# Optimization experiments

Measured on AMD Instinct MI355X. Metric: run time of the kernel, lower is better.

The kernel has to match this reference:

```python
import jax, jax.numpy as jnp
import numpy as np

B, S, D, H = 4, 2048, 1024, 16
HD = D // H  # head_dim = 64


def setup_inputs() -> dict:
    key = jax.random.key(0)
    ks = jax.random.split(key, 6)
    scale = 1.0 / np.sqrt(D)
    x = jax.random.normal(ks[0], (B, S, D), dtype=jnp.float32)
    mask = jax.random.bernoulli(ks[1], 0.9, (B, S, S))  # bool, True = keep
    wq = jax.random.normal(ks[2], (D, D), dtype=jnp.float32) * scale
    wk = jax.random.normal(ks[3], (D, D), dtype=jnp.float32) * scale
    wv = jax.random.normal(ks[4], (D, D), dtype=jnp.float32) * scale
    wo = jax.random.normal(ks[5], (D, D), dtype=jnp.float32) * scale
    return {"x": x, "mask": mask, "wq": wq, "wk": wk, "wv": wv, "wo": wo}


def reference(x, mask, wq, wk, wv, wo):
    bsz, seqlen, dim = x.shape
    # nn.Linear applies x @ W.T; weights here stored as [out, in]
    xq = (x @ wq.T).reshape(bsz, seqlen, H, HD)
    xk = (x @ wk.T).reshape(bsz, seqlen, H, HD)
    xv = (x @ wv.T).reshape(bsz, seqlen, H, HD)
    # scores: [B, H, S, S]
    scores = jnp.einsum("bqhd,bkhd->bhqk", xq, xk) / np.sqrt(HD).astype(np.float32)
    # additive mask: ~mask * -1e9, broadcast over heads
    neg = jnp.where(mask[:, None, :, :], 0.0, -1e9).astype(scores.dtype)
    scores = scores + neg
    scores = jax.nn.softmax(scores.astype(jnp.float32), axis=-1).astype(xq.dtype)
    # multiplicative re-mask after softmax (as in the original)
    scores = scores * mask[:, None, :, :].astype(scores.dtype)
    out = jnp.einsum("bhqk,bkhd->bqhd", scores, xv).reshape(bsz, seqlen, dim)
    return out @ wo.T
```

## Files before the change

### kernel.cpp

```cpp
#include <hip/hip_runtime.h>
#include <hip/hip_bf16.h>

#define S_LEN 2048
#define DIM   1024
#define NHEAD 16
#define HDIM  64
#define QSCALE 0.18033688f

typedef __attribute__((ext_vector_type(8))) short bfrag;
typedef __attribute__((ext_vector_type(4))) float f32x4;
typedef __attribute__((ext_vector_type(16))) float f32x16;
typedef __attribute__((ext_vector_type(4))) unsigned int u32x4;

#define MFMA(a,b,c)   __builtin_amdgcn_mfma_f32_16x16x32_bf16((a),(b),(c),0,0,0)
#define MFMA32(a,b,c) __builtin_amdgcn_mfma_f32_32x32x16_bf16((a),(b),(c),0,0,0)

__device__ __forceinline__ unsigned short f2bf(float x) {
  __hip_bfloat16 h = __float2bfloat16(x);
  return *reinterpret_cast<unsigned short*>(&h);
}

__device__ __forceinline__ unsigned int pk2bf(float a, float b) {
  float2 f2; f2.x = a; f2.y = b;
  __hip_bfloat162 b2 = __float22bfloat162_rn(f2);
  return *reinterpret_cast<unsigned int*>(&b2);
}

__device__ __forceinline__ void gll16(const unsigned short* g, unsigned short* l) {
  __builtin_amdgcn_global_load_lds(
      (const __attribute__((address_space(1))) unsigned int*)g,
      (__attribute__((address_space(3))) unsigned int*)l, 16, 0, 0);
}

__global__ void probe(const unsigned int* __restrict__ x,
                      const unsigned int* __restrict__ mask,
                      int* __restrict__ flags) {
  const int lane = threadIdx.x;
  int insane = 0;
  for (int i = lane; i < 512; i += 64) {
    unsigned int w = x[i];
    unsigned int e = (w >> 7) & 0xFFu;
    bool sane = (e >= 90u && e <= 160u) || ((w & 0x7FFFu) == 0u);
    insane += sane ? 0 : 1;
  }
  bool all01 = true, allu8 = true, allf32 = true, allbf = true;
  for (int i = lane; i < 1024; i += 64) {
    unsigned int w = mask[i];
    all01  &= (w <= 1u);
    allu8  &= ((w & 0xFEFEFEFEu) == 0u);
    allf32 &= (w == 0u || w == 0x3F800000u);
    unsigned int lo = w & 0xFFFFu, hi = w >> 16;
    allbf  &= (lo == 0u || lo == 0x3F80u) && (hi == 0u || hi == 0x3F80u);
  }
#pragma unroll
  for (int off = 1; off < 64; off <<= 1) insane += __shfl_xor(insane, off, 64);
  const unsigned long long full = ~0ull;
  const bool g01  = __ballot(all01)  == full;
  const bool gu8  = __ballot(allu8)  == full;
  const bool gf32 = __ballot(allf32) == full;
  const bool gbf  = __ballot(allbf)  == full;
  if (lane == 0) {
    flags[0] = (insane > 128) ? 1 : 0;
    flags[1] = g01 ? 1 : (gu8 ? 0 : (gf32 ? 2 : (gbf ? 3 : 0)));
  }
}

__device__ __forceinline__ bool mask_at(const void* mk, int mode, size_t idx) {
  switch (mode) {
    case 0:  return ((const unsigned char*)mk)[idx]  != 0;
    case 1:  return ((const int*)mk)[idx]            != 0;
    case 2:  return ((const unsigned int*)mk)[idx]   != 0u;
    default: return ((const unsigned short*)mk)[idx] != 0;
  }
}

__global__ __launch_bounds__(256) void cvt_all(
    const void* __restrict__ x,  const void* __restrict__ wq,
    const void* __restrict__ wk, const void* __restrict__ wv,
    const void* __restrict__ wo,
    unsigned short* __restrict__ xb,  unsigned short* __restrict__ wqb,
    unsigned short* __restrict__ wkb, unsigned short* __restrict__ wvb,
    unsigned short* __restrict__ wob, const int* __restrict__ flags) {
  const int bx = blockIdx.x;
  const void* src; unsigned short* dst; int i;
  if (bx < 4096) { src = x; dst = xb; i = bx * 256 + threadIdx.x; }
  else {
    const int r = (bx - 4096) >> 9, off = (bx - 4096) & 511;
    src = r == 0 ? wq : r == 1 ? wk : r == 2 ? wv : wo;
    dst = r == 0 ? wqb : r == 1 ? wkb : r == 2 ? wvb : wob;
    i = off * 256 + threadIdx.x;
  }
  if (flags[0]) {
    const float* p = (const float*)src + (size_t)i * 8;
    float4 a = *reinterpret_cast<const float4*>(p);
    float4 b = *reinterpret_cast<const float4*>(p + 4);
    unsigned int d0 = pk2bf(a.x, a.y), d1 = pk2bf(a.z, a.w);
    unsigned int d2 = pk2bf(b.x, b.y), d3 = pk2bf(b.z, b.w);
    uint4 o; o.x = d0; o.y = d1; o.z = d2; o.w = d3;
    *reinterpret_cast<uint4*>(dst + (size_t)i * 8) = o;
  } else {
    *reinterpret_cast<bfrag*>(dst + (size_t)i * 8) =
        reinterpret_cast<const bfrag*>(src)[i];
  }
}

__global__ __launch_bounds__(256) void bitmask(const void* __restrict__ mk,
                                               const int* __restrict__ flags,
                                               unsigned long long* __restrict__ mb) {
  size_t gid = (size_t)blockIdx.x * 256 + threadIdx.x;
  bool v = mask_at(mk, flags[1], gid);
  unsigned long long w = __ballot(v);
  if ((threadIdx.x & 63) == 0) {
    const size_t bb = gid >> 22;
    const size_t q  = (gid >> 11) & 2047;
    const size_t wd = (gid >> 6) & 31;
    mb[(bb * 32 + wd) * 2048 + q] = w;
  }
}

__global__ __launch_bounds__(256) void gemm128(const unsigned short* __restrict__ A,
                                               const unsigned short* __restrict__ Bt,
                                               void* __restrict__ C,
                                               const int* __restrict__ flags,
                                               int aHsplit, int cMode) {
  __shared__ unsigned short As[128 * 64];
  __shared__ unsigned short Bs[128 * 64];
  const int t = threadIdx.x, lane = t & 63, wave = t >> 6;
  const int r16 = lane & 15, quad = lane >> 4;

  const int nwgx = gridDim.x;
  const int nwg  = nwgx * gridDim.y;
  const int orig = blockIdx.y * nwgx + blockIdx.x;
  const int cpx  = nwg >> 3;
  const int swz  = (orig & 7) * cpx + (orig >> 3);
  const int n0 = (swz % nwgx) * 128, m0 = (swz / nwgx) * 128;

  const int wm = (wave >> 1) * 64, wn = (wave & 1) * 64;
  const int srow = t >> 3;
  const int sgr  = (t & 7) ^ (srow & 7);

  f32x4 acc[4][4];
#pragma unroll
  for (int i = 0; i < 4; ++i)
#pragma unroll
    for (int j = 0; j < 4; ++j) acc[i][j] = (f32x4){0.f, 0.f, 0.f, 0.f};

  for (int k0 = 0; k0 < 1024; k0 += 64) {
    __syncthreads();
#pragma unroll
    for (int rr = 0; rr < 4; ++rr) {
      const int row = rr * 32 + srow;
      const int m = m0 + row;
      const int k = k0 + sgr * 8;
      const unsigned short* ga;
      if (aHsplit) ga = A + ((size_t)(((m >> 11) << 4) + (k >> 6)) * 2048 + (m & 2047)) * 64 + (k & 63);
      else         ga = A + (size_t)m * 1024 + k;
      gll16(ga, As + rr * 2048 + wave * 512);
      const unsigned short* gb = Bt + (size_t)(n0 + row) * 1024 + k;
      gll16(gb, Bs + rr * 2048 + wave * 512);
    }
    __syncthreads();

#pragma unroll
    for (int kk = 0; kk < 2; ++kk) {
      bfrag af[4], bf[4];
#pragma unroll
      for (int i = 0; i < 4; ++i)
        af[i] = *reinterpret_cast<const bfrag*>(
            &As[(wm + i * 16 + r16) * 64 + (((kk * 4 + quad) ^ (r16 & 7)) * 8)]);
#pragma unroll
      for (int j = 0; j < 4; ++j)
        bf[j] = *reinterpret_cast<const bfrag*>(
            &Bs[(wn + j * 16 + r16) * 64 + (((kk * 4 + quad) ^ (r16 & 7)) * 8)]);
#pragma unroll
      for (int i = 0; i < 4; ++i)
#pragma unroll
        for (int j = 0; j < 4; ++j)
          acc[i][j] = MFMA(af[i], bf[j], acc[i][j]);
    }
  }

  const int oF = (cMode == 2) ? flags[0] : 0;
#pragma unroll
  for (int i = 0; i < 4; ++i)
#pragma unroll
    for (int j = 0; j < 4; ++j)
#pragma unroll
      for (int r = 0; r < 4; ++r) {
        const int m = m0 + wm + i * 16 + quad * 4 + r;
        const int n = n0 + wn + j * 16 + r16;
        const float v = acc[i][j][r];
        if (cMode == 3) {
          const int region = n >> 10, nn = n & 1023;
          const float vv = (region == 0) ? v * QSCALE : v;
          const size_t idx = (size_t)region * 8388608 +
              ((size_t)((m >> 11) * NHEAD + (nn >> 6)) * 2048 + (m & 2047)) * 64 + (nn & 63);
          ((unsigned short*)C)[idx] = f2bf(vv);
        } else if (cMode == 1) {
          const size_t idx = ((size_t)((m >> 11) * NHEAD + (n >> 6)) * 2048 + (m & 2047)) * 64 + (n & 63);
          ((unsigned short*)C)[idx] = f2bf(v);
        } else {
          const size_t idx = (size_t)m * 1024 + n;
          if (oF) ((float*)C)[idx] = v;
          else    ((unsigned short*)C)[idx] = f2bf(v);
        }
      }
}

__global__ __launch_bounds__(256) void transposeV(const unsigned short* __restrict__ xvH,
                                                  unsigned short* __restrict__ xvT) {
  __shared__ unsigned short Ts[64 * 80];
  const int t = threadIdx.x;
  const int s0 = blockIdx.x * 64, bh = blockIdx.y;
  const int sr = t >> 3, seg = (t & 7) * 8;
#pragma unroll
  for (int rr = 0; rr < 2; ++rr) {
    const int s = rr * 32 + sr;
    bfrag v = *reinterpret_cast<const bfrag*>(xvH + ((size_t)bh * 2048 + s0 + s) * 64 + seg);
#pragma unroll
    for (int j = 0; j < 8; ++j) Ts[(seg + j) * 80 + s] = (unsigned short)v[j];
  }
  __syncthreads();
#pragma unroll
  for (int rr = 0; rr < 2; ++rr) {
    const int d = rr * 32 + sr;
    bfrag o = *reinterpret_cast<const bfrag*>(&Ts[d * 80 + seg]);
    *reinterpret_cast<bfrag*>(xvT + ((size_t)bh * 64 + d) * 2048 + s0 + seg) = o;
  }
}

#if defined(__has_builtin)
#if __has_builtin(__builtin_amdgcn_permlane32_swap)
#define HAVE_PL32_SWAP 1
#endif
#endif
#ifndef HAVE_PL32_SWAP
#define HAVE_PL32_SWAP 0
#endif

__global__ __launch_bounds__(256, 3) void fattn(const unsigned short* __restrict__ qH,
                                                const unsigned short* __restrict__ kH,
                                                const unsigned short* __restrict__ vT,
                                                const unsigned long long* __restrict__ mbT,
                                                unsigned short* __restrict__ oH) {
  __shared__ unsigned short Ks[2][64 * 64];
  __shared__ unsigned short Vs[2][64 * 64];
  const int t = threadIdx.x, lane = t & 63, wave = t >> 6;
  const int l31 = lane & 31, hi = lane >> 5;
  const int bid = blockIdx.x;
  const int bh = bid & 63, qidx = bid >> 6;
  const int b = bh >> 4;
  const int qw = qidx * 128 + wave * 32;
  const size_t hbase = (size_t)bh * S_LEN;
  const int kgr = l31 & 7;

  bfrag qf[4];
#pragma unroll
  for (int s = 0; s < 4; ++s)
    qf[s] = *reinterpret_cast<const bfrag*>(
        qH + (hbase + qw + l31) * 64 + s * 16 + hi * 8);

  f32x16 o0, o1;
#pragma unroll
  for (int r = 0; r < 16; ++r) { o0[r] = 0.f; o1[r] = 0.f; }
  float ls[4] = {0.f, 0.f, 0.f, 0.f};

  const int srow = lane >> 3;
  const int sg   = (lane & 7) ^ srow;

  auto stage = [&](int buf, int kb) {
#pragma unroll
    for (int rr = 0; rr < 2; ++rr) {
      const int row = rr * 32 + wave * 8 + srow;
      gll16(kH + (hbase + kb + row) * 64 + sg * 8, &Ks[buf][rr * 2048 + wave * 512]);
      gll16(vT + ((size_t)bh * 64 + row) * 2048 + kb + sg * 8, &Vs[buf][rr * 2048 + wave * 512]);
    }
  };

  stage(0, 0);
  int cur = 0;
  const unsigned long long* mcol = mbT + (size_t)b * 32 * S_LEN + (qw + l31);
  unsigned long long wcur = mcol[0];

  for (int kb = 0; kb < S_LEN; kb += 64) {
    __syncthreads();
    const bool more = (kb + 64 < S_LEN);
    if (more) stage(cur ^ 1, kb + 64);
    const unsigned long long wnext =
        more ? mcol[(size_t)((kb >> 6) + 1) * S_LEN] : 0ull;

    const unsigned int wlo = (unsigned int)(wcur >> (4 * hi));
    const unsigned int whi = (unsigned int)(wcur >> (32 + 4 * hi));

#pragma unroll
    for (int c = 0; c < 2; ++c) {
      f32x16 z;
#pragma unroll
      for (int r = 0; r < 16; ++r) z[r] = 0.f;
      __builtin_amdgcn_s_setprio(1);
#pragma unroll
      for (int s = 0; s < 4; ++s) {
        const int gr = (2 * s + hi) ^ kgr;
        bfrag kf = *reinterpret_cast<const bfrag*>(
            &Ks[cur][(c * 32 + l31) * 64 + gr * 8]);
        z = MFMA32(kf, qf[s], z);
      }
      __builtin_amdgcn_s_setprio(0);
      const unsigned int wm = c ? whi : wlo;

#pragma unroll
      for (int s2 = 0; s2 < 2; ++s2) {
        float e[8];
#pragma unroll
        for (int j = 0; j < 8; ++j) {
          const int r = 8 * s2 + j;
          const int bitp = (r & 3) + 8 * (r >> 2);
          float ev = __builtin_amdgcn_exp2f(z[r]);
          ev = (wm & (1u << bitp)) ? ev : 0.f;
          e[j] = ev;
          ls[r & 3] += ev;
        }
        const unsigned int pwa = pk2bf(e[0], e[1]);
        const unsigned int pwb = pk2bf(e[2], e[3]);
        const unsigned int pwc = pk2bf(e[4], e[5]);
        const unsigned int pwd = pk2bf(e[6], e[7]);
        u32x4 uu;
#if HAVE_PL32_SWAP
        auto r02 = __builtin_amdgcn_permlane32_swap(pwa, pwc, false, false);
        auto r13 = __builtin_amdgcn_permlane32_swap(pwb, pwd, false, false);
        uu.x = r02[0];
        uu.y = r13[0];
        uu.z = r02[1];
        uu.w = r13[1];
#else
        const unsigned int t0 = __shfl_xor(pwa, 32, 64);
        const unsigned int t1 = __shfl_xor(pwb, 32, 64);
        const unsigned int t2 = __shfl_xor(pwc, 32, 64);
        const unsigned int t3 = __shfl_xor(pwd, 32, 64);
        uu.x = hi ? t2 : pwa;
        uu.y = hi ? t3 : pwb;
        uu.z = hi ? pwc : t0;
        uu.w = hi ? pwd : t1;
#endif
        const bfrag pf = __builtin_bit_cast(bfrag, uu);
        const int s = 2 * c + s2;
        const int gv = (2 * s + hi) ^ kgr;
        bfrag v0 = *reinterpret_cast<const bfrag*>(&Vs[cur][l31 * 64 + gv * 8]);
        bfrag v1 = *reinterpret_cast<const bfrag*>(&Vs[cur][(32 + l31) * 64 + gv * 8]);
        __builtin_amdgcn_s_setprio(1);
        o0 = MFMA32(pf, v0, o0);
        o1 = MFMA32(pf, v1, o1);
        __builtin_amdgcn_s_setprio(0);
      }
    }
    wcur = wnext;
    cur ^= 1;
  }

  float lsum = (ls[0] + ls[1]) + (ls[2] + ls[3]);
  lsum += __shfl_xor(lsum, 32, 64);
  const float inv = 1.f / fmaxf(lsum, 1e-30f);
#pragma unroll
  for (int r = 0; r < 16; ++r) {
    const int qr = (r & 3) + 8 * (r >> 2) + 4 * hi;
    const float sc = __shfl(inv, qr, 64);
    unsigned short* op = oH + (hbase + qw + qr) * 64 + l31;
    op[0]  = f2bf(o0[r] * sc);
    op[32] = f2bf(o1[r] * sc);
  }
}

template<bool F32>
__device__ __forceinline__ bfrag load8(const void* base, size_t idx) {
  if constexpr (F32) {
    const float* p = (const float*)base + idx;
    float4 u = *reinterpret_cast<const float4*>(p);
    float4 v = *reinterpret_cast<const float4*>(p + 4);
    bfrag r;
    r[0]=(short)f2bf(u.x); r[1]=(short)f2bf(u.y); r[2]=(short)f2bf(u.z); r[3]=(short)f2bf(u.w);
    r[4]=(short)f2bf(v.x); r[5]=(short)f2bf(v.y); r[6]=(short)f2bf(v.z); r[7]=(short)f2bf(v.w);
    return r;
  } else {
    return *reinterpret_cast<const bfrag*>((const unsigned short*)base + idx);
  }
}

template<bool AF32, bool BF32>
__device__ __forceinline__ void gemm_body(const void* __restrict__ A, const void* __restrict__ Bt,
                                          void* __restrict__ C, int N, int K, bool outF32) {
  const int lane = threadIdx.x & 63, wave = threadIdx.x >> 6;
  const int r16 = lane & 15, quad = lane >> 4;
  const int m0 = (blockIdx.y * 4 + wave) * 16, n0 = blockIdx.x * 64;
  f32x4 acc[4];
#pragma unroll
  for (int i = 0; i < 4; ++i) acc[i] = (f32x4){0.f,0.f,0.f,0.f};
  const size_t aoff = (size_t)(m0 + r16) * K + quad * 8;
  const size_t boff = (size_t)(n0 + r16) * K + quad * 8;
  for (int k0 = 0; k0 < K; k0 += 32) {
    bfrag a = load8<AF32>(A, aoff + k0);
#pragma unroll
    for (int tt = 0; tt < 4; ++tt) {
      bfrag bb = load8<BF32>(Bt, boff + (size_t)tt * 16 * K + k0);
      acc[tt] = MFMA(a, bb, acc[tt]);
    }
  }
#pragma unroll
  for (int tt = 0; tt < 4; ++tt)
#pragma unroll
    for (int r = 0; r < 4; ++r) {
      const size_t ci = (size_t)(m0 + quad * 4 + r) * N + n0 + tt * 16 + r16;
      if (outF32) ((float*)C)[ci] = acc[tt][r];
      else        ((unsigned short*)C)[ci] = f2bf(acc[tt][r]);
    }
}

__global__ __launch_bounds__(256) void gemm_bt(const void* A, const void* Bt, void* C,
                                               int N, int K, const int* flags,
                                               int aFollows, int outFollows) {
  const int f = flags[0];
  const bool aF = (aFollows != 0) && (f != 0);
  const bool oF = (outFollows != 0) && (f != 0);
  if (f) { if (aF) gemm_body<true, true>(A, Bt, C, N, K, oF);
           else    gemm_body<false, true>(A, Bt, C, N, K, oF); }
  else     gemm_body<false, false>(A, Bt, C, N, K, oF);
}

__global__ __launch_bounds__(64) void fattn_r2(const unsigned short* __restrict__ xq,
                                               const unsigned short* __restrict__ xk,
                                               const unsigned short* __restrict__ xv,
                                               const void* __restrict__ mk,
                                               const int* __restrict__ flags,
                                               unsigned short* __restrict__ xo) {
  __shared__ unsigned short smemP[16 * 32];
  const int lane = threadIdx.x, r16 = lane & 15, quad = lane >> 4;
  const int q0 = blockIdx.x * 16, h = blockIdx.y, b = blockIdx.z;
  const int mmode = flags[1];
  const size_t base = (size_t)b * S_LEN * DIM + (size_t)h * HDIM;
  const size_t mbase = (size_t)b * S_LEN * S_LEN;
  bfrag aq0 = *reinterpret_cast<const bfrag*>(xq + base + (size_t)(q0 + r16) * DIM + quad * 8);
  bfrag aq1 = *reinterpret_cast<const bfrag*>(xq + base + (size_t)(q0 + r16) * DIM + 32 + quad * 8);
  f32x4 o[4];
#pragma unroll
  for (int i = 0; i < 4; ++i) o[i] = (f32x4){0.f,0.f,0.f,0.f};
  float m_r[4] = {-1e30f,-1e30f,-1e30f,-1e30f}, l_r[4] = {0.f,0.f,0.f,0.f};
  for (int kb = 0; kb < S_LEN; kb += 32) {
    const unsigned short* k0p = xk + base + (size_t)(kb + r16) * DIM + quad * 8;
    const unsigned short* k1p = k0p + (size_t)16 * DIM;
    f32x4 s0 = (f32x4){0.f,0.f,0.f,0.f}, s1 = (f32x4){0.f,0.f,0.f,0.f};
    s0 = MFMA(aq0, *reinterpret_cast<const bfrag*>(k0p), s0);
    s0 = MFMA(aq1, *reinterpret_cast<const bfrag*>(k0p + 32), s0);
    s1 = MFMA(aq0, *reinterpret_cast<const bfrag*>(k1p), s1);
    s1 = MFMA(aq1, *reinterpret_cast<const bfrag*>(k1p + 32), s1);
    float l0[4], l1[4], tmax[4];
#pragma unroll
    for (int r = 0; r < 4; ++r) {
      const size_t mrow = mbase + (size_t)(q0 + quad * 4 + r) * S_LEN + kb;
      l0[r] = mask_at(mk, mmode, mrow + r16) ? s0[r] * 0.125f : -1e30f;
      l1[r] = mask_at(mk, mmode, mrow + 16 + r16) ? s1[r] * 0.125f : -1e30f;
      tmax[r] = fmaxf(l0[r], l1[r]);
    }
#pragma unroll
    for (int off = 1; off < 16; off <<= 1)
#pragma unroll
      for (int r = 0; r < 4; ++r) tmax[r] = fmaxf(tmax[r], __shfl_xor(tmax[r], off, 64));
    float p0[4], p1[4], rsum[4];
#pragma unroll
    for (int r = 0; r < 4; ++r) {
      const float mnew = fmaxf(m_r[r], tmax[r]);
      const float alpha = __expf(m_r[r] - mnew);
      m_r[r] = mnew;
      p0[r] = (l0[r] <= -1e29f) ? 0.f : __expf(l0[r] - mnew);
      p1[r] = (l1[r] <= -1e29f) ? 0.f : __expf(l1[r] - mnew);
      rsum[r] = p0[r] + p1[r];
      l_r[r] *= alpha;
#pragma unroll
      for (int tt = 0; tt < 4; ++tt) o[tt][r] *= alpha;
    }
#pragma unroll
    for (int off = 1; off < 16; off <<= 1)
#pragma unroll
      for (int r = 0; r < 4; ++r) rsum[r] += __shfl_xor(rsum[r], off, 64);
#pragma unroll
    for (int r = 0; r < 4; ++r) l_r[r] += rsum[r];
#pragma unroll
    for (int r = 0; r < 4; ++r) {
      smemP[(quad * 4 + r) * 32 + r16] = f2bf(p0[r]);
      smemP[(quad * 4 + r) * 32 + 16 + r16] = f2bf(p1[r]);
    }
    __syncthreads();
    bfrag apf = *reinterpret_cast<const bfrag*>(&smemP[r16 * 32 + quad * 8]);
    const unsigned short* vbase = xv + base + (size_t)(kb + quad * 8) * DIM + r16;
#pragma unroll
    for (int tt = 0; tt < 4; ++tt) {
      bfrag bv;
#pragma unroll
      for (int j = 0; j < 8; ++j) bv[j] = (short)vbase[(size_t)j * DIM + tt * 16];
      o[tt] = MFMA(apf, bv, o[tt]);
    }
    __syncthreads();
  }
#pragma unroll
  for (int tt = 0; tt < 4; ++tt)
#pragma unroll
    for (int r = 0; r < 4; ++r)
      xo[base + (size_t)(q0 + quad * 4 + r) * DIM + tt * 16 + r16] = f2bf(o[tt][r] / l_r[r]);
}

extern "C" void kernel_launch(void* const* d_in, const int* in_sizes, int n_in,
                              void* d_out, int out_size, void* d_ws, size_t ws_size,
                              hipStream_t stream) {
  const void* x  = d_in[0];
  const void* mk = d_in[1];
  const void* wq = d_in[2];
  const void* wk = d_in[3];
  const void* wv = d_in[4];
  const void* wo = d_in[5];

  const size_t MiB = 1048576;
  const size_t NEED = 4096 + 90 * MiB;

  if (ws_size >= NEED) {
    char* p = (char*)d_ws;
    int* flags = (int*)p;                       p += 4096;
    unsigned short* xb  = (unsigned short*)p;   p += 16 * MiB;
    unsigned short* wqb = (unsigned short*)p;   p += 2 * MiB;
    unsigned short* wkb = (unsigned short*)p;   p += 2 * MiB;
    unsigned short* wvb = (unsigned short*)p;   p += 2 * MiB;
    unsigned short* wob = (unsigned short*)p;   p += 2 * MiB;
    unsigned long long* mb = (unsigned long long*)p; p += 2 * MiB;
    unsigned short* xqH = (unsigned short*)p;   p += 16 * MiB;
    unsigned short* xkH = (unsigned short*)p;   p += 16 * MiB;
    unsigned short* xvH = (unsigned short*)p;   p += 16 * MiB;
    unsigned short* xvT = (unsigned short*)p;   p += 16 * MiB;
    unsigned short* xoH = xvH;

    probe<<<1, 64, 0, stream>>>((const unsigned int*)x, (const unsigned int*)mk, flags);
    cvt_all<<<6144, 256, 0, stream>>>(x, wq, wk, wv, wo, xb, wqb, wkb, wvb, wob, flags);
    bitmask<<<65536, 256, 0, stream>>>(mk, flags, mb);

    gemm128<<<dim3(24, 64), 256, 0, stream>>>(xb, wqb, xqH, flags, 0, 3);
    transposeV<<<dim3(32, 64), 256, 0, stream>>>(xvH, xvT);
    fattn<<<dim3(1024), 256, 0, stream>>>(xqH, xkH, xvT, mb, xoH);
    gemm128<<<dim3(8, 64), 256, 0, stream>>>(xoH, wob, d_out, flags, 1, 2);
  } else {
    int* flags = (int*)d_ws;
    unsigned short* xq = (unsigned short*)((char*)d_ws + 256);
    unsigned short* xk = xq + (size_t)8388608;
    unsigned short* xv = xk + (size_t)8388608;
    unsigned short* xo = xv + (size_t)8388608;
    probe<<<1, 64, 0, stream>>>((const unsigned int*)x, (const unsigned int*)mk, flags);
    dim3 gg(16, 128);
    gemm_bt<<<gg, 256, 0, stream>>>(x, wq, xq, 1024, 1024, flags, 1, 0);
    gemm_bt<<<gg, 256, 0, stream>>>(x, wk, xk, 1024, 1024, flags, 1, 0);
    gemm_bt<<<gg, 256, 0, stream>>>(x, wv, xv, 1024, 1024, flags, 1, 0);
    fattn_r2<<<dim3(128, NHEAD, 4), 64, 0, stream>>>(xq, xk, xv, mk, flags, xo);
    gemm_bt<<<gg, 256, 0, stream>>>(xo, wo, d_out, 1024, 1024, flags, 0, 1);
  }
}
```

Measured before the change: 383.6 us.

## Fuse V transpose into QKV GEMM epilogue and batch QK^T MFMAs

The QKV projection epilogue now writes the V region directly in transposed [bh, d, s] layout with 4-element vector stores, so the separate transposeV kernel and its 16 MiB round trip are dropped. In the attention kernel both 32-row score tiles are computed back-to-back before the softmax/PV stages, giving more independent MFMAs to interleave. The cost is a strided transposed store pattern in the GEMM epilogue and higher register pressure in fattn from holding two score accumulators.

```diff
diff --git a/kernel.cpp b/kernel.cpp
--- a/kernel.cpp
+++ b/kernel.cpp
@@ -184,49 +184,40 @@
 #pragma unroll
   for (int i = 0; i < 4; ++i)
 #pragma unroll
-    for (int j = 0; j < 4; ++j)
-#pragma unroll
-      for (int r = 0; r < 4; ++r) {
-        const int m = m0 + wm + i * 16 + quad * 4 + r;
-        const int n = n0 + wn + j * 16 + r16;
-        const float v = acc[i][j][r];
-        if (cMode == 3) {
-          const int region = n >> 10, nn = n & 1023;
-          const float vv = (region == 0) ? v * QSCALE : v;
-          const size_t idx = (size_t)region * 8388608 +
-              ((size_t)((m >> 11) * NHEAD + (nn >> 6)) * 2048 + (m & 2047)) * 64 + (nn & 63);
-          ((unsigned short*)C)[idx] = f2bf(vv);
-        } else if (cMode == 1) {
-          const size_t idx = ((size_t)((m >> 11) * NHEAD + (n >> 6)) * 2048 + (m & 2047)) * 64 + (n & 63);
-          ((unsigned short*)C)[idx] = f2bf(v);
-        } else {
-          const size_t idx = (size_t)m * 1024 + n;
-          if (oF) ((float*)C)[idx] = v;
-          else    ((unsigned short*)C)[idx] = f2bf(v);
+    for (int j = 0; j < 4; ++j) {
+      const int mb = m0 + wm + i * 16 + quad * 4;
+      const int n  = n0 + wn + j * 16 + r16;
+      if (cMode == 3 && (n >> 10) == 2) {
+        const int nn = n & 1023;
+        const int bh = (mb >> 11) * NHEAD + (nn >> 6);
+        const size_t idx = (size_t)2 * 8388608 +
+            ((size_t)bh * 64 + (nn & 63)) * 2048 + (mb & 2047);
+        ushort4 o;
+        o.x = f2bf(acc[i][j][0]); o.y = f2bf(acc[i][j][1]);
+        o.z = f2bf(acc[i][j][2]); o.w = f2bf(acc[i][j][3]);
+        *reinterpret_cast<ushort4*>((unsigned short*)C + idx) = o;
+      } else {
+#pragma unroll
+        for (int r = 0; r < 4; ++r) {
+          const int m = mb + r;
+          const float v = acc[i][j][r];
+          if (cMode == 3) {
+            const int region = n >> 10, nn = n & 1023;
+            const float vv = (region == 0) ? v * QSCALE : v;
+            const size_t idx = (size_t)region * 8388608 +
+                ((size_t)((m >> 11) * NHEAD + (nn >> 6)) * 2048 + (m & 2047)) * 64 + (nn & 63);
+            ((unsigned short*)C)[idx] = f2bf(vv);
+          } else if (cMode == 1) {
+            const size_t idx = ((size_t)((m >> 11) * NHEAD + (n >> 6)) * 2048 + (m & 2047)) * 64 + (n & 63);
+            ((unsigned short*)C)[idx] = f2bf(v);
+          } else {
+            const size_t idx = (size_t)m * 1024 + n;
+            if (oF) ((float*)C)[idx] = v;
+            else    ((unsigned short*)C)[idx] = f2bf(v);
+          }
         }
       }
-}
-
-__global__ __launch_bounds__(256) void transposeV(const unsigned short* __restrict__ xvH,
-                                                  unsigned short* __restrict__ xvT) {
-  __shared__ unsigned short Ts[64 * 80];
-  const int t = threadIdx.x;
-  const int s0 = blockIdx.x * 64, bh = blockIdx.y;
-  const int sr = t >> 3, seg = (t & 7) * 8;
-#pragma unroll
-  for (int rr = 0; rr < 2; ++rr) {
-    const int s = rr * 32 + sr;
-    bfrag v = *reinterpret_cast<const bfrag*>(xvH + ((size_t)bh * 2048 + s0 + s) * 64 + seg);
-#pragma unroll
-    for (int j = 0; j < 8; ++j) Ts[(seg + j) * 80 + s] = (unsigned short)v[j];
-  }
-  __syncthreads();
-#pragma unroll
-  for (int rr = 0; rr < 2; ++rr) {
-    const int d = rr * 32 + sr;
-    bfrag o = *reinterpret_cast<const bfrag*>(&Ts[d * 80 + seg]);
-    *reinterpret_cast<bfrag*>(xvT + ((size_t)bh * 64 + d) * 2048 + s0 + seg) = o;
-  }
+    }
 }
 
 #if defined(__has_builtin)
@@ -282,6 +273,53 @@
   const unsigned long long* mcol = mbT + (size_t)b * 32 * S_LEN + (qw + l31);
   unsigned long long wcur = mcol[0];
 
+  auto smpv = [&](const f32x16& z, unsigned int wm, int c) {
+#pragma unroll
+    for (int s2 = 0; s2 < 2; ++s2) {
+      float e[8];
+#pragma unroll
+      for (int j = 0; j < 8; ++j) {
+        const int r = 8 * s2 + j;
+        const int bitp = (r & 3) + 8 * (r >> 2);
+        float ev = __builtin_amdgcn_exp2f(z[r]);
+        ev = (wm & (1u << bitp)) ? ev : 0.f;
+        e[j] = ev;
+        ls[r & 3] += ev;
+      }
+      const unsigned int pwa = pk2bf(e[0], e[1]);
+      const unsigned int pwb = pk2bf(e[2], e[3]);
+      const unsigned int pwc = pk2bf(e[4], e[5]);
+      const unsigned int pwd = pk2bf(e[6], e[7]);
+      u32x4 uu;
+#if HAVE_PL32_SWAP
+      auto r02 = __builtin_amdgcn_permlane32_swap(pwa, pwc, false, false);
+      auto r13 = __builtin_amdgcn_permlane32_swap(pwb, pwd, false, false);
+      uu.x = r02[0];
+      uu.y = r13[0];
+      uu.z = r02[1];
+      uu.w = r13[1];
+#else
+      const unsigned int t0 = __shfl_xor(pwa, 32, 64);
+      const unsigned int t1 = __shfl_xor(pwb, 32, 64);
+      const unsigned int t2 = __shfl_xor(pwc, 32, 64);
+      const unsigned int t3 = __shfl_xor(pwd, 32, 64);
+      uu.x = hi ? t2 : pwa;
+      uu.y = hi ? t3 : pwb;
+      uu.z = hi ? pwc : t0;
+      uu.w = hi ? pwd : t1;
+#endif
+      const bfrag pf = __builtin_bit_cast(bfrag, uu);
+      const int s = 2 * c + s2;
+      const int gv = (2 * s + hi) ^ kgr;
+      bfrag v0 = *reinterpret_cast<const bfrag*>(&Vs[cur][l31 * 64 + gv * 8]);
+      bfrag v1 = *reinterpret_cast<const bfrag*>(&Vs[cur][(32 + l31) * 64 + gv * 8]);
+      __builtin_amdgcn_s_setprio(1);
+      o0 = MFMA32(pf, v0, o0);
+      o1 = MFMA32(pf, v1, o1);
+      __builtin_amdgcn_s_setprio(0);
+    }
+  };
+
   for (int kb = 0; kb < S_LEN; kb += 64) {
     __syncthreads();
     const bool more = (kb + 64 < S_LEN);
@@ -292,67 +330,23 @@
     const unsigned int wlo = (unsigned int)(wcur >> (4 * hi));
     const unsigned int whi = (unsigned int)(wcur >> (32 + 4 * hi));
 
-#pragma unroll
-    for (int c = 0; c < 2; ++c) {
-      f32x16 z;
-#pragma unroll
-      for (int r = 0; r < 16; ++r) z[r] = 0.f;
-      __builtin_amdgcn_s_setprio(1);
-#pragma unroll
-      for (int s = 0; s < 4; ++s) {
-        const int gr = (2 * s + hi) ^ kgr;
-        bfrag kf = *reinterpret_cast<const bfrag*>(
-            &Ks[cur][(c * 32 + l31) * 64 + gr * 8]);
-        z = MFMA32(kf, qf[s], z);
-      }
-      __builtin_amdgcn_s_setprio(0);
-      const unsigned int wm = c ? whi : wlo;
-
-#pragma unroll
-      for (int s2 = 0; s2 < 2; ++s2) {
-        float e[8];
-#pragma unroll
-        for (int j = 0; j < 8; ++j) {
-          const int r = 8 * s2 + j;
-          const int bitp = (r & 3) + 8 * (r >> 2);
-          float ev = __builtin_amdgcn_exp2f(z[r]);
-          ev = (wm & (1u << bitp)) ? ev : 0.f;
-          e[j] = ev;
-          ls[r & 3] += ev;
-        }
-        const unsigned int pwa = pk2bf(e[0], e[1]);
-        const unsigned int pwb = pk2bf(e[2], e[3]);
-        const unsigned int pwc = pk2bf(e[4], e[5]);
-        const unsigned int pwd = pk2bf(e[6], e[7]);
-        u32x4 uu;
-#if HAVE_PL32_SWAP
-        auto r02 = __builtin_amdgcn_permlane32_swap(pwa, pwc, false, false);
-        auto r13 = __builtin_amdgcn_permlane32_swap(pwb, pwd, false, false);
-        uu.x = r02[0];
-        uu.y = r13[0];
-        uu.z = r02[1];
-        uu.w = r13[1];
-#else
-        const unsigned int t0 = __shfl_xor(pwa, 32, 64);
-        const unsigned int t1 = __shfl_xor(pwb, 32, 64);
-        const unsigned int t2 = __shfl_xor(pwc, 32, 64);
-        const unsigned int t3 = __shfl_xor(pwd, 32, 64);
-        uu.x = hi ? t2 : pwa;
-        uu.y = hi ? t3 : pwb;
-        uu.z = hi ? pwc : t0;
-        uu.w = hi ? pwd : t1;
-#endif
-        const bfrag pf = __builtin_bit_cast(bfrag, uu);
-        const int s = 2 * c + s2;
-        const int gv = (2 * s + hi) ^ kgr;
-        bfrag v0 = *reinterpret_cast<const bfrag*>(&Vs[cur][l31 * 64 + gv * 8]);
-        bfrag v1 = *reinterpret_cast<const bfrag*>(&Vs[cur][(32 + l31) * 64 + gv * 8]);
-        __builtin_amdgcn_s_setprio(1);
-        o0 = MFMA32(pf, v0, o0);
-        o1 = MFMA32(pf, v1, o1);
-        __builtin_amdgcn_s_setprio(0);
-      }
-    }
+    f32x16 z0, z1;
+#pragma unroll
+    for (int r = 0; r < 16; ++r) { z0[r] = 0.f; z1[r] = 0.f; }
+    __builtin_amdgcn_s_setprio(1);
+#pragma unroll
+    for (int s = 0; s < 4; ++s) {
+      const int gr = (2 * s + hi) ^ kgr;
+      bfrag kf0 = *reinterpret_cast<const bfrag*>(&Ks[cur][l31 * 64 + gr * 8]);
+      bfrag kf1 = *reinterpret_cast<const bfrag*>(&Ks[cur][(32 + l31) * 64 + gr * 8]);
+      z0 = MFMA32(kf0, qf[s], z0);
+      z1 = MFMA32(kf1, qf[s], z1);
+    }
+    __builtin_amdgcn_s_setprio(0);
+
+    smpv(z0, wlo, 0);
+    smpv(z1, whi, 1);
+
     wcur = wnext;
     cur ^= 1;
   }
@@ -530,16 +524,15 @@
     unsigned long long* mb = (unsigned long long*)p; p += 2 * MiB;
     unsigned short* xqH = (unsigned short*)p;   p += 16 * MiB;
     unsigned short* xkH = (unsigned short*)p;   p += 16 * MiB;
-    unsigned short* xvH = (unsigned short*)p;   p += 16 * MiB;
     unsigned short* xvT = (unsigned short*)p;   p += 16 * MiB;
-    unsigned short* xoH = xvH;
+    unsigned short* xoH = (unsigned short*)p;   p += 16 * MiB;
+    (void)xkH; (void)xvT;
 
     probe<<<1, 64, 0, stream>>>((const unsigned int*)x, (const unsigned int*)mk, flags);
     cvt_all<<<6144, 256, 0, stream>>>(x, wq, wk, wv, wo, xb, wqb, wkb, wvb, wob, flags);
     bitmask<<<65536, 256, 0, stream>>>(mk, flags, mb);
 
     gemm128<<<dim3(24, 64), 256, 0, stream>>>(xb, wqb, xqH, flags, 0, 3);
-    transposeV<<<dim3(32, 64), 256, 0, stream>>>(xvH, xvT);
     fattn<<<dim3(1024), 256, 0, stream>>>(xqH, xkH, xvT, mb, xoH);
     gemm128<<<dim3(8, 64), 256, 0, stream>>>(xoH, wob, d_out, flags, 1, 2);
   } else {
```

Result: faster. 373.6 us (-2.6%).
